# Performance work log

Hardware: AMD Instinct MI355X
Metric: run time of the kernel (lower is better)

## Reference

```python
import jax, jax.numpy as jnp
import numpy as np

NUM_BINS = 16
TAU = 0.05
EPS_SUM = 1e-8
EPS_LOG = 1e-10


def _entropy(counts):
    # counts: (dim, bins) -> (dim,) entropy in bits
    probs = counts / jnp.clip(counts.sum(axis=-1, keepdims=True), EPS_SUM, None)
    return -(probs * jnp.log2(probs + EPS_LOG)).sum(axis=-1)


def setup_inputs() -> dict:
    key = jax.random.key(0)
    k1, k2 = jax.random.split(key)
    dim = 2097152
    observation = jax.random.normal(k1, (8, dim), dtype=jnp.float32)
    # positive histogram counts (buffer starts at ones in torch; randomize for a nontrivial test)
    belief_counts = jax.random.uniform(k2, (dim, NUM_BINS), dtype=jnp.float32)
    return {"observation": observation, "belief_counts": belief_counts}


def reference(observation, belief_counts):
    if observation.ndim == 2:
        observation = observation.mean(axis=0)  # (dim,)
    dim = observation.shape[0]

    prior_probs = belief_counts / jnp.clip(
        belief_counts.sum(axis=-1, keepdims=True), EPS_SUM, None)

    # sigmoid binning -> int bin indices in [0, NUM_BINS-1]
    normalized = jax.nn.sigmoid(observation)
    bins = jnp.clip((normalized * (NUM_BINS - 1)).astype(jnp.int32), 0, NUM_BINS - 1)

    one_hot = jax.nn.one_hot(bins, NUM_BINS, dtype=belief_counts.dtype)  # (dim, bins)
    posterior_counts = belief_counts + one_hot
    posterior_probs = posterior_counts / jnp.clip(
        posterior_counts.sum(axis=-1, keepdims=True), EPS_SUM, None)

    H_prior = _entropy(belief_counts)
    H_posterior = _entropy(posterior_counts)

    info_gain = jnp.clip(
        (posterior_probs * jnp.log2((posterior_probs + EPS_LOG) / (prior_probs + EPS_LOG))).sum(axis=-1),
        0.0, None)
    mean_info_gain = info_gain.mean()
    epistemic_value = jax.nn.sigmoid(mean_info_gain * 50.0 - 1.0)

    # EMA buffer update (no_grad in torch)
    new_belief_counts = jnp.clip(belief_counts * (1.0 - TAU) + one_hot * TAU, 0.01, None)

    return (info_gain, mean_info_gain, H_prior, H_posterior, epistemic_value,
            new_belief_counts)
```

## Files before the change

### kernel.cpp

```cpp
#include <hip/hip_runtime.h>
#include <math.h>

namespace {
constexpr int   NUM_BINS = 16;
constexpr float TAU      = 0.05f;
constexpr float EPS_SUM  = 1e-8f;
constexpr float EPS_LOG  = 1e-10f;
constexpr int   BLOCK    = 256;
constexpr int   GRID     = 2048;
}

__global__ __launch_bounds__(BLOCK) void ev_main(
    const float* __restrict__ obs,
    const float* __restrict__ belief,
    float* __restrict__ out_info,
    float* __restrict__ out_Hprior,
    float* __restrict__ out_Hpost,
    float* __restrict__ out_newbelief,
    float* __restrict__ ws_partials,
    int dim)
{
    float local_sum = 0.0f;
    const int stride = BLOCK * GRID;
    for (int r = blockIdx.x * BLOCK + threadIdx.x; r < dim; r += stride) {
        float c[NUM_BINS];
        const float4* bp = reinterpret_cast<const float4*>(belief) + (size_t)r * 4;
        float4 v0 = bp[0];
        float4 v1 = bp[1];
        float4 v2 = bp[2];
        float4 v3 = bp[3];
        c[0]=v0.x;  c[1]=v0.y;  c[2]=v0.z;  c[3]=v0.w;
        c[4]=v1.x;  c[5]=v1.y;  c[6]=v1.z;  c[7]=v1.w;
        c[8]=v2.x;  c[9]=v2.y;  c[10]=v2.z; c[11]=v2.w;
        c[12]=v3.x; c[13]=v3.y; c[14]=v3.z; c[15]=v3.w;

        float s = 0.0f;
#pragma unroll
        for (int j = 0; j < NUM_BINS; ++j) s += c[j];

        float om = 0.0f;
#pragma unroll
        for (int k = 0; k < 8; ++k) om += obs[(size_t)k * dim + r];
        om *= 0.125f;

        float sig = 1.0f / (1.0f + expf(-om));
        int bin = (int)(sig * 15.0f);
        bin = bin < 0 ? 0 : (bin > 15 ? 15 : bin);

        float inv_prior = 1.0f / fmaxf(s, EPS_SUM);
        float inv_post  = 1.0f / fmaxf(s + 1.0f, EPS_SUM);

        float Hpr = 0.0f, Hpo = 0.0f, ig = 0.0f;
        float nb[NUM_BINS];
#pragma unroll
        for (int j = 0; j < NUM_BINS; ++j) {
            float cj = c[j];
            float oh = (j == bin) ? 1.0f : 0.0f;
            float p  = cj * inv_prior;
            float pp = (cj + oh) * inv_post;
            float lp  = log2f(p  + EPS_LOG);
            float lpp = log2f(pp + EPS_LOG);
            Hpr -= p  * lp;
            Hpo -= pp * lpp;
            ig  += pp * (lpp - lp);
            nb[j] = fmaxf(cj * (1.0f - TAU) + oh * TAU, 0.01f);
        }
        ig = fmaxf(ig, 0.0f);
        local_sum += ig;

        out_info[r]   = ig;
        out_Hprior[r] = Hpr;
        out_Hpost[r]  = Hpo;

        float2* nbp = reinterpret_cast<float2*>(out_newbelief) + (size_t)r * 8;
#pragma unroll
        for (int j = 0; j < 8; ++j)
            nbp[j] = make_float2(nb[2*j], nb[2*j + 1]);
    }

    __shared__ float sdata[BLOCK];
    sdata[threadIdx.x] = local_sum;
    __syncthreads();
#pragma unroll
    for (int off = BLOCK / 2; off > 0; off >>= 1) {
        if (threadIdx.x < off) sdata[threadIdx.x] += sdata[threadIdx.x + off];
        __syncthreads();
    }
    if (threadIdx.x == 0) ws_partials[blockIdx.x] = sdata[0];
}

__global__ __launch_bounds__(BLOCK) void ev_finalize(
    const float* __restrict__ ws_partials,
    float* __restrict__ out_mean,
    float* __restrict__ out_epi,
    int n_partials, float inv_dim)
{
    float s = 0.0f;
    for (int i = threadIdx.x; i < n_partials; i += BLOCK) s += ws_partials[i];
    __shared__ float sdata[BLOCK];
    sdata[threadIdx.x] = s;
    __syncthreads();
#pragma unroll
    for (int off = BLOCK / 2; off > 0; off >>= 1) {
        if (threadIdx.x < off) sdata[threadIdx.x] += sdata[threadIdx.x + off];
        __syncthreads();
    }
    if (threadIdx.x == 0) {
        float mean = sdata[0] * inv_dim;
        *out_mean = mean;
        *out_epi  = 1.0f / (1.0f + expf(-(mean * 50.0f - 1.0f)));
    }
}

extern "C" void kernel_launch(void* const* d_in, const int* in_sizes, int n_in,
                              void* d_out, int out_size, void* d_ws, size_t ws_size,
                              hipStream_t stream)
{
    const float* obs    = (const float*)d_in[0];
    const float* belief = (const float*)d_in[1];
    const int dim = in_sizes[0] / 8;

    float* o             = (float*)d_out;
    float* out_info      = o;
    float* out_mean      = o + dim;
    float* out_Hprior    = o + dim + 1;
    float* out_Hpost     = o + 2 * (size_t)dim + 1;
    float* out_epi       = o + 3 * (size_t)dim + 1;
    float* out_newbelief = o + 3 * (size_t)dim + 2;

    float* partials = (float*)d_ws;

    ev_main<<<GRID, BLOCK, 0, stream>>>(obs, belief, out_info, out_Hprior,
                                        out_Hpost, out_newbelief, partials, dim);
    ev_finalize<<<1, BLOCK, 0, stream>>>(partials, out_mean, out_epi, GRID,
                                         1.0f / (float)dim);
}
```

Baseline: 322.0 us.

## Split each histogram row across a quad of lanes with DPP reductions

Each row of 16 bins is now handled by four adjacent lanes, each taking one float4 of counts and two of the eight observation rows. Row sums, observation means and entropy and info-gain partials are combined with DPP quad shuffles. The aim is fully coalesced belief loads and new-belief stores across a wavefront instead of each lane striding 64 bytes, plus more parallelism. In exchange the sigmoid and reciprocals are computed redundantly in every lane, the scalar outputs are written by only one lane in four, and the mean divisor becomes 4*dim because every lane adds the row's gain.

After: 316.6 us. Within noise of the previous version (-1.7%).

```diff
diff --git a/kernel.cpp b/kernel.cpp
--- a/kernel.cpp
+++ b/kernel.cpp
@@ -10,6 +10,14 @@
 constexpr int   GRID     = 2048;
 }
 
+__device__ inline float quad_sum(float x) {
+    int a = __builtin_amdgcn_mov_dpp(__float_as_int(x), 0xB1, 0xF, 0xF, true);
+    x += __int_as_float(a);
+    a = __builtin_amdgcn_mov_dpp(__float_as_int(x), 0x4E, 0xF, 0xF, true);
+    x += __int_as_float(a);
+    return x;
+}
+
 __global__ __launch_bounds__(BLOCK) void ev_main(
     const float* __restrict__ obs,
     const float* __restrict__ belief,
@@ -20,42 +28,43 @@
     float* __restrict__ ws_partials,
     int dim)
 {
+    const int tid    = blockIdx.x * BLOCK + threadIdx.x;
+    const int stride = BLOCK * GRID;
+    const int W      = dim * 4;
     float local_sum = 0.0f;
-    const int stride = BLOCK * GRID;
-    for (int r = blockIdx.x * BLOCK + threadIdx.x; r < dim; r += stride) {
-        float c[NUM_BINS];
-        const float4* bp = reinterpret_cast<const float4*>(belief) + (size_t)r * 4;
-        float4 v0 = bp[0];
-        float4 v1 = bp[1];
-        float4 v2 = bp[2];
-        float4 v3 = bp[3];
-        c[0]=v0.x;  c[1]=v0.y;  c[2]=v0.z;  c[3]=v0.w;
-        c[4]=v1.x;  c[5]=v1.y;  c[6]=v1.z;  c[7]=v1.w;
-        c[8]=v2.x;  c[9]=v2.y;  c[10]=v2.z; c[11]=v2.w;
-        c[12]=v3.x; c[13]=v3.y; c[14]=v3.z; c[15]=v3.w;
 
-        float s = 0.0f;
-#pragma unroll
-        for (int j = 0; j < NUM_BINS; ++j) s += c[j];
+    const float4* belief4 = reinterpret_cast<const float4*>(belief);
+    float2* nb2 = reinterpret_cast<float2*>(out_newbelief);
 
-        float om = 0.0f;
-#pragma unroll
-        for (int k = 0; k < 8; ++k) om += obs[(size_t)k * dim + r];
-        om *= 0.125f;
+#pragma unroll 2
+    for (int f = tid; f < W; f += stride) {
+        const int r = f >> 2;
+        const int m = f & 3;
+
+        float4 c4 = belief4[f];
+        float cs = (c4.x + c4.y) + (c4.z + c4.w);
+        float os = obs[(size_t)(2 * m) * dim + r]
+                 + obs[(size_t)(2 * m + 1) * dim + r];
+
+        cs = quad_sum(cs);
+        os = quad_sum(os);
+        float om = os * 0.125f;
 
         float sig = 1.0f / (1.0f + expf(-om));
         int bin = (int)(sig * 15.0f);
         bin = bin < 0 ? 0 : (bin > 15 ? 15 : bin);
 
-        float inv_prior = 1.0f / fmaxf(s, EPS_SUM);
-        float inv_post  = 1.0f / fmaxf(s + 1.0f, EPS_SUM);
+        float inv_prior = 1.0f / fmaxf(cs, EPS_SUM);
+        float inv_post  = 1.0f / fmaxf(cs + 1.0f, EPS_SUM);
 
         float Hpr = 0.0f, Hpo = 0.0f, ig = 0.0f;
-        float nb[NUM_BINS];
+        float cc[4] = {c4.x, c4.y, c4.z, c4.w};
+        float nb[4];
+        const int j0 = m * 4;
 #pragma unroll
-        for (int j = 0; j < NUM_BINS; ++j) {
-            float cj = c[j];
-            float oh = (j == bin) ? 1.0f : 0.0f;
+        for (int e = 0; e < 4; ++e) {
+            float cj = cc[e];
+            float oh = (j0 + e == bin) ? 1.0f : 0.0f;
             float p  = cj * inv_prior;
             float pp = (cj + oh) * inv_post;
             float lp  = log2f(p  + EPS_LOG);
@@ -63,19 +72,21 @@
             Hpr -= p  * lp;
             Hpo -= pp * lpp;
             ig  += pp * (lpp - lp);
-            nb[j] = fmaxf(cj * (1.0f - TAU) + oh * TAU, 0.01f);
+            nb[e] = fmaxf(cj * (1.0f - TAU) + oh * TAU, 0.01f);
         }
-        ig = fmaxf(ig, 0.0f);
+        Hpr = quad_sum(Hpr);
+        Hpo = quad_sum(Hpo);
+        ig  = fmaxf(quad_sum(ig), 0.0f);
         local_sum += ig;
 
-        out_info[r]   = ig;
-        out_Hprior[r] = Hpr;
-        out_Hpost[r]  = Hpo;
+        if (m == 0) {
+            out_info[r]   = ig;
+            out_Hprior[r] = Hpr;
+            out_Hpost[r]  = Hpo;
+        }
 
-        float2* nbp = reinterpret_cast<float2*>(out_newbelief) + (size_t)r * 8;
-#pragma unroll
-        for (int j = 0; j < 8; ++j)
-            nbp[j] = make_float2(nb[2*j], nb[2*j + 1]);
+        nb2[(size_t)f * 2]     = make_float2(nb[0], nb[1]);
+        nb2[(size_t)f * 2 + 1] = make_float2(nb[2], nb[3]);
     }
 
     __shared__ float sdata[BLOCK];
@@ -93,7 +104,7 @@
     const float* __restrict__ ws_partials,
     float* __restrict__ out_mean,
     float* __restrict__ out_epi,
-    int n_partials, float inv_dim)
+    int n_partials, float inv_cnt)
 {
     float s = 0.0f;
     for (int i = threadIdx.x; i < n_partials; i += BLOCK) s += ws_partials[i];
@@ -106,7 +117,7 @@
         __syncthreads();
     }
     if (threadIdx.x == 0) {
-        float mean = sdata[0] * inv_dim;
+        float mean = sdata[0] * inv_cnt;
         *out_mean = mean;
         *out_epi  = 1.0f / (1.0f + expf(-(mean * 50.0f - 1.0f)));
     }
@@ -133,5 +144,5 @@
     ev_main<<<GRID, BLOCK, 0, stream>>>(obs, belief, out_info, out_Hprior,
                                         out_Hpost, out_newbelief, partials, dim);
     ev_finalize<<<1, BLOCK, 0, stream>>>(partials, out_mean, out_epi, GRID,
-                                         1.0f / (float)dim);
+                                         1.0f / (4.0f * (float)dim));
 }
```
